# Kernel tuning notes

Measured on AMD Instinct MI355X. Metric: run time of the kernel, lower is better.

## Reference

```python
import jax, jax.numpy as jnp
import numpy as np

H = 256   # hidden_size
D = 256   # embedding_dim
C = 111   # num_classes


def _pos_encoding(L, d):
    pos = jnp.arange(L, dtype=jnp.float32)[:, None]
    div = jnp.exp(jnp.arange(0, d, 2, dtype=jnp.float32) * (-np.log(10000.0) / d))
    pe = jnp.zeros((L, d), dtype=jnp.float32)
    pe = pe.at[:, 0::2].set(jnp.sin(pos * div))
    pe = pe.at[:, 1::2].set(jnp.cos(pos * div))
    return pe


def setup_inputs() -> dict:
    key = jax.random.key(0)
    ks = jax.random.split(key, 12)
    B, Cin, Hh, Ww, T = 64, 1024, 16, 64, 64
    s = 0.02
    return {
        "feature_map": jax.random.normal(ks[0], (B, Cin, Hh, Ww), jnp.float32),
        "count_vector": jax.random.uniform(ks[1], (B, C), jnp.float32),
        "target": jax.random.randint(ks[2], (B, T), 0, C),
        "conv_w": jax.random.normal(ks[3], (2 * H, Cin), jnp.float32) * s,
        "conv_b": jnp.zeros((2 * H,), jnp.float32),
        "emb": jax.random.normal(ks[4], (C, D), jnp.float32) * s,
        "gru_wih": jax.random.normal(ks[5], (3 * H, D + H + C), jnp.float32) * s,
        "gru_whh": jax.random.normal(ks[6], (3 * H, H), jnp.float32) * s,
        "gru_bih": jnp.zeros((3 * H,), jnp.float32),
        "gru_bhh": jnp.zeros((3 * H,), jnp.float32),
        "attn_w": jax.random.normal(ks[7], (H, 2 * H), jnp.float32) * s,
        "attn_b": jnp.zeros((H,), jnp.float32),
        "attn_v": jax.random.normal(ks[8], (1, H), jnp.float32) * s,
        "attn_vb": jnp.zeros((1,), jnp.float32),
        "cov_w": jax.random.normal(ks[9], (H, 1), jnp.float32) * s,
        "cov_b": jnp.zeros((H,), jnp.float32),
        "out_w": jax.random.normal(ks[10], (C, 2 * H + C), jnp.float32) * s,
        "out_b": jnp.zeros((C,), jnp.float32),
    }


def reference(feature_map, count_vector, target, conv_w, conv_b, emb,
              gru_wih, gru_whh, gru_bih, gru_bhh, attn_w, attn_b,
              attn_v, attn_vb, cov_w, cov_b, out_w, out_b):
    B, _, hh, ww = feature_map.shape
    L = hh * ww
    # 1x1 conv + permute to (B, h, w, 2H), add positional encoding, flatten
    feats = jnp.einsum('bchw,oc->bhwo', feature_map, conv_w) + conv_b
    pe = _pos_encoding(L, 2 * H).reshape(hh, ww, 2 * H)
    feats = (feats + pe[None]).reshape(B, L, 2 * H)
    # attention_w(projected_features) is time-invariant -> hoist out of the loop
    Wf = jnp.einsum('bld,hd->blh', feats, attn_w) + attn_b  # (B, L, H)

    # teacher forcing with ratio 1.0: inputs are <sos>=1 then target[:, :-1]
    y_in = jnp.concatenate([jnp.ones((B, 1), target.dtype), target[:, :-1]], axis=1)

    def gru_cell(x, h):  # PyTorch GRUCell math
        gi = x @ gru_wih.T + gru_bih
        gh = h @ gru_whh.T + gru_bhh
        i_r, i_z, i_n = jnp.split(gi, 3, axis=-1)
        h_r, h_z, h_n = jnp.split(gh, 3, axis=-1)
        r = jax.nn.sigmoid(i_r + h_r)
        z = jax.nn.sigmoid(i_z + h_z)
        n = jnp.tanh(i_n + r * h_n)
        return (1.0 - z) * n + z * h

    def step(carry, y_t):
        h, cov = carry  # h: (B,H), cov: (B,L)
        embedded = emb[y_t]
        a = jnp.tanh(Wf + cov[:, :, None] * cov_w[:, 0] + cov_b + h[:, None, :])
        scores = jnp.einsum('blh,h->bl', a, attn_v[0]) + attn_vb[0]
        alpha = jax.nn.softmax(scores, axis=1)
        cov = cov + alpha
        context = jnp.einsum('bl,bld->bd', alpha, feats)[:, :H]
        x = jnp.concatenate([embedded, context, count_vector], axis=1)
        h = gru_cell(x, h)
        out_t = jnp.concatenate([h, context, count_vector], axis=1) @ out_w.T + out_b
        return (h, cov), out_t

    h0 = jnp.zeros((B, H), feats.dtype)
    cov0 = jnp.zeros((B, L), feats.dtype)
    _, outs = jax.lax.scan(step, (h0, cov0), y_in.T)  # (T, B, C)
    return jnp.transpose(outs, (1, 0, 2))
```

## Files before the change

### kernel.cpp

```cpp
#include <hip/hip_runtime.h>
#include <hip/hip_bf16.h>
#include <cstdint>
#include <cstddef>

#define B_   64
#define CIN  1024
#define L_   1024
#define T_   64
#define Hh_  256
#define Dd_  256
#define Cc_  111
#define NO_  512
#define KX_  623

typedef __attribute__((ext_vector_type(8))) short short8;
typedef __attribute__((ext_vector_type(4))) float floatx4;

__device__ __forceinline__ float bf2f(unsigned short u) {
    union { unsigned int i; float f; } v; v.i = ((unsigned int)u) << 16; return v.f;
}
__device__ __forceinline__ unsigned short f2bf(float f) {
    union { float f; unsigned int i; } v; v.f = f;
    return (unsigned short)((v.i + 0x7fffu + ((v.i >> 16) & 1u)) >> 16);
}
__device__ __forceinline__ float frcp(float x) { return __builtin_amdgcn_rcpf(x); }
__device__ __forceinline__ float tanh_fast(float x) {
    return 1.0f - 2.0f * frcp(1.0f + __expf(2.0f * x));
}
__device__ __forceinline__ float sig_fast(float x) {
    return frcp(1.0f + __expf(-x));
}


__global__ void pe_kernel(float* __restrict__ PE) {
    int idx = blockIdx.x * 256 + threadIdx.x;
    if (idx >= L_ * NO_) return;
    int l = idx >> 9, j = idx & 511;
    int i2 = j & ~1;
    float div = expf((float)i2 * (-9.210340371976184f / 512.0f));
    float arg = (float)l * div;
    PE[idx] = (j & 1) ? cosf(arg) : sinf(arg);
}

__global__ void wc_kernel(const float* __restrict__ conv_w,
                          const float* __restrict__ attn_w,
                          unsigned short* __restrict__ Wc) {
    int c = blockIdx.x * 256 + threadIdx.x;
    int o = blockIdx.y;
    float v;
    if (o < 256) {
        v = conv_w[(size_t)o * CIN + c];
    } else {
        const float* aw = attn_w + (size_t)(o - 256) * 512;
        float a = 0.0f;
        for (int d = 0; d < 512; ++d)
            a = fmaf(aw[d], conv_w[(size_t)d * CIN + c], a);
        v = a;
    }
    Wc[(size_t)o * CIN + c] = f2bf(v);
}

__global__ void biasf_kernel(const float* __restrict__ conv_b,
                             const float* __restrict__ PE,
                             float* __restrict__ biasC) {
    int idx = blockIdx.x * 256 + threadIdx.x;
    int l = idx >> 8, j = idx & 255;
    biasC[(size_t)l * NO_ + j] = conv_b[j] + PE[(size_t)l * NO_ + j];
}

__global__ void biasw_kernel(const float* __restrict__ conv_b,
                             const float* __restrict__ PE,
                             const float* __restrict__ attn_w,
                             const float* __restrict__ attn_b,
                             float* __restrict__ biasC) {
    int l = blockIdx.x * 256 + threadIdx.x;
    int h = blockIdx.y;
    const float* aw = attn_w + (size_t)h * 512;
    const float* pe = PE + (size_t)l * NO_;
    float a = 0.0f;
    for (int d = 0; d < 512; ++d)
        a = fmaf(aw[d], conv_b[d] + pe[d], a);
    biasC[(size_t)l * NO_ + 256 + h] = a + attn_b[h];
}

__global__ void wiht_kernel(const float* __restrict__ wih, unsigned short* __restrict__ WihT) {
    int idx = blockIdx.x * 256 + threadIdx.x;
    if (idx >= 768 * KX_) return;
    int o = idx / KX_, k = idx - o * KX_;
    WihT[(size_t)k * 768 + o] = f2bf(wih[idx]);
}
__global__ void whht_kernel(const float* __restrict__ whh, unsigned short* __restrict__ WhhT) {
    int idx = blockIdx.x * 256 + threadIdx.x;
    if (idx >= 768 * 256) return;
    int o = idx >> 8, k = idx & 255;
    WhhT[(size_t)k * 768 + o] = f2bf(whh[idx]);
}
__global__ void woutt_kernel(const float* __restrict__ outw, unsigned short* __restrict__ WoutT) {
    int idx = blockIdx.x * 256 + threadIdx.x;
    if (idx >= Cc_ * KX_) return;
    int c = idx / KX_, k = idx - c * KX_;
    WoutT[(size_t)k * 128 + c] = f2bf(outw[idx]);
}

__global__ void zero_kernel(int* __restrict__ p, int n) {
    int i = blockIdx.x * 256 + threadIdx.x;
    if (i < n) p[i] = 0;
}

__global__ __launch_bounds__(256) void gemm_feats(
    const float* __restrict__ fm,
    const unsigned short* __restrict__ Wc,
    const float* __restrict__ biasC,
    unsigned short* __restrict__ F) {
    __shared__ __align__(16) unsigned short Als[128 * 40];
    __shared__ __align__(16) unsigned short Bls[128 * 40];
    const int tid  = threadIdx.x;
    const int bx   = blockIdx.x;
    const int bb   = bx >> 3;
    const int l0   = (bx & 7) << 7;
    const int n0   = blockIdx.y << 7;
    const int wid  = tid >> 6;
    const int lane = tid & 63;
    const int m0w  = (wid & 1) << 6;
    const int n0w  = (wid >> 1) << 6;
    const int quad = lane >> 4;
    const int l16  = lane & 15;

    floatx4 acc[4][4];
#pragma unroll
    for (int i = 0; i < 4; ++i)
#pragma unroll
        for (int j = 0; j < 4; ++j)
            acc[i][j] = (floatx4){0.f, 0.f, 0.f, 0.f};

    const int lt    = tid & 127;
    const int chalf = tid >> 7;
    const float* fmb = fm + ((size_t)bb * CIN) * L_ + l0 + lt;
    const int bo = tid >> 2;
    const int bc = (tid & 3) << 3;
    const int swzA = ((lt >> 2) & 3) << 3;

    for (int kk = 0; kk < 32; ++kk) {
        const int c0 = kk << 5;
        __syncthreads();
#pragma unroll
        for (int i = 0; i < 8; ++i) {
            int cc = (chalf + (i << 1)) << 1;
            float v0 = fmb[(size_t)(c0 + cc) * L_];
            float v1 = fmb[(size_t)(c0 + cc + 1) * L_];
            unsigned int pk = (unsigned int)f2bf(v0) | ((unsigned int)f2bf(v1) << 16);
            *(unsigned int*)(&Als[lt * 40 + (cc ^ swzA)]) = pk;
        }
#pragma unroll
        for (int i = 0; i < 2; ++i) {
            int o = bo + (i << 6);
            uint4 w = *(const uint4*)(&Wc[(size_t)(n0 + o) * CIN + c0 + bc]);
            *(uint4*)(&Bls[o * 40 + bc]) = w;
        }
        __syncthreads();
        short8 afr[4], bfr[4];
#pragma unroll
        for (int mf = 0; mf < 4; ++mf) {
            int mm = m0w + (mf << 4) + l16;
            int k0 = (quad << 3) ^ (((mm >> 2) & 3) << 3);
            afr[mf] = *(const short8*)(&Als[mm * 40 + k0]);
        }
#pragma unroll
        for (int nf = 0; nf < 4; ++nf) {
            int nn = n0w + (nf << 4) + l16;
            bfr[nf] = *(const short8*)(&Bls[nn * 40 + (quad << 3)]);
        }
#pragma unroll
        for (int mf = 0; mf < 4; ++mf)
#pragma unroll
            for (int nf = 0; nf < 4; ++nf)
                acc[mf][nf] = __builtin_amdgcn_mfma_f32_16x16x32_bf16(afr[mf], bfr[nf], acc[mf][nf], 0, 0, 0);
    }

#pragma unroll
    for (int mf = 0; mf < 4; ++mf) {
#pragma unroll
        for (int nf = 0; nf < 4; ++nf) {
            int colg = n0 + n0w + (nf << 4) + l16;
#pragma unroll
            for (int r = 0; r < 4; ++r) {
                int lb = l0 + m0w + (mf << 4) + (quad << 2) + r;
                float v = acc[mf][nf][r] + biasC[(size_t)lb * NO_ + colg];
                F[((size_t)bb * L_ + lb) * NO_ + colg] = f2bf(v);
            }
        }
    }
}


__device__ __forceinline__ void batch_barrier(int* bar, int target, int tid) {
    __syncthreads();
    if (tid == 0) {
        __hip_atomic_fetch_add(bar, 1, __ATOMIC_RELEASE, __HIP_MEMORY_SCOPE_AGENT);
        while (__hip_atomic_load(bar, __ATOMIC_ACQUIRE, __HIP_MEMORY_SCOPE_AGENT) < target) {
            __builtin_amdgcn_s_sleep(2);
        }
    }
    __syncthreads();
}

__global__ __launch_bounds__(1024, 4) void decoder_kernel(
    const unsigned short* __restrict__ F,
    const unsigned short* __restrict__ WihT,
    const unsigned short* __restrict__ WhhT,
    const unsigned short* __restrict__ WoutT,
    const float* __restrict__ cvv,
    const int* __restrict__ tgt,
    const float* __restrict__ emb,
    const float* __restrict__ bih,
    const float* __restrict__ bhh,
    const float* __restrict__ attn_v,
    const float* __restrict__ attn_vb,
    const float* __restrict__ cov_w,
    const float* __restrict__ cov_b,
    const float* __restrict__ outb,
    int* __restrict__ bar,
    float* __restrict__ gsum,
    float* __restrict__ gctx,
    float* __restrict__ ggih,
    float* __restrict__ OUT) {
    __shared__ __align__(16) unsigned short Wls[256 * 256];
    __shared__ float sc[256];
    __shared__ float cov[256];
    __shared__ float xv[640];
    __shared__ float xo[640];
    __shared__ float hv[256];
    __shared__ __align__(16) float hbs[256];
    __shared__ __align__(16) float cwls[256];
    __shared__ __align__(16) float avls[256];
    __shared__ float gi[768];
    __shared__ float gh[768];
    __shared__ float ctxp[2048];
    __shared__ float outp[1024];
    __shared__ float red[32];

    const int tid  = threadIdx.x;
    const int bx   = blockIdx.x;
    const int b    = bx >> 2;
    const int sub  = bx & 3;
    const int l0   = sub << 8;
    const int lane = tid & 63;
    const int wid  = tid >> 6;
    const int l16  = tid & 15;
    const int lg   = tid >> 4;

    int* mybar = bar + b * 16;

    if (tid < 256) {
        cov[tid] = 0.0f; hv[tid] = 0.0f; hbs[tid] = cov_b[tid];
        cwls[tid] = cov_w[tid]; avls[tid] = attn_v[tid];
    }
    if (tid >= 512 && tid < 512 + Cc_) xv[tid] = cvv[b * Cc_ + (tid - 512)];

    const float avb = attn_vb[0];

#pragma unroll
    for (int i = 0; i < 8; ++i) {
        int c   = (i << 10) + tid;
        int row = c >> 5;
        int col = (c & 31) << 3;
        *(uint4*)(&Wls[(row << 8) + col]) =
            *(const uint4*)(F + (((size_t)(b * L_ + l0 + row)) << 9) + Hh_ + col);
    }

    unsigned int fctx[32];
    {
        const int hp = (tid & 127) << 1;
        const int ch = tid >> 7;
        const unsigned short* fb = F + (((size_t)(b * L_ + l0 + (ch << 5))) << 9) + hp;
#pragma unroll
        for (int i = 0; i < 32; ++i)
            fctx[i] = *(const unsigned int*)(fb + ((size_t)i << 9));
    }

    const int cbase = sub * 28;
    const int ccnt  = (sub == 3) ? 27 : 28;
    const int kg0 = sub * 156;
    const int kg1 = (kg0 + 156 > KX_) ? KX_ : kg0 + 156;
    const int kh0 = sub << 6;

    int nsync = 0;
    __syncthreads();

    for (int t = 0; t < T_; ++t) {
        const int par = t & 1;
        float* myctx = gctx + (((size_t)b * 2 + par) * 4) * 256;
        float* mysum = gsum + ((size_t)b * 2 + par) * 4;
        float* mygg  = ggih + (((size_t)b * 2 + par) * 4) * 1536;

        if (tid < 256) {
            int ytok = (t == 0) ? 1 : tgt[b * T_ + t - 1];
            xv[tid] = emb[ytok * Dd_ + tid];
        }

#pragma unroll
        for (int pass = 0; pass < 4; ++pass) {
            int ll = (pass << 6) + lg;
            float covl = cov[ll];
            const unsigned short* wf = &Wls[ll << 8];
            float a = 0.0f;
#pragma unroll
            for (int j = 0; j < 4; ++j) {
                const int hb0 = (j << 6) + (l16 << 2);
                uint2 w = *(const uint2*)(wf + hb0);
                float4 cw4 = *(const float4*)(&cwls[hb0]);
                float4 av4 = *(const float4*)(&avls[hb0]);
                float4 hb4 = *(const float4*)(&hbs[hb0]);
                float g0 = bf2f((unsigned short)(w.x & 0xffffu)) + fmaf(covl, cw4.x, hb4.x);
                float g1 = bf2f((unsigned short)(w.x >> 16))     + fmaf(covl, cw4.y, hb4.y);
                float g2 = bf2f((unsigned short)(w.y & 0xffffu)) + fmaf(covl, cw4.z, hb4.z);
                float g3 = bf2f((unsigned short)(w.y >> 16))     + fmaf(covl, cw4.w, hb4.w);
                a = fmaf(av4.x, tanh_fast(g0), a);
                a = fmaf(av4.y, tanh_fast(g1), a);
                a = fmaf(av4.z, tanh_fast(g2), a);
                a = fmaf(av4.w, tanh_fast(g3), a);
            }
            a += __shfl_xor(a, 1);
            a += __shfl_xor(a, 2);
            a += __shfl_xor(a, 4);
            a += __shfl_xor(a, 8);
            if (l16 == 0) sc[ll] = __expf(a + avb);
        }
        __syncthreads();

        if (tid < 256) {
            float e = sc[tid];
#pragma unroll
            for (int off = 1; off < 64; off <<= 1) e += __shfl_xor(e, off);
            if (lane == 0) red[wid] = e;
        }

        {
            int hp = (tid & 127) << 1;
            int ch = tid >> 7;
            float c0a = 0.0f, c1a = 0.0f;
#pragma unroll
            for (int i = 0; i < 32; ++i) {
                float al = sc[(ch << 5) + i];
                unsigned int w = fctx[i];
                c0a = fmaf(al, bf2f((unsigned short)(w & 0xffffu)), c0a);
                c1a = fmaf(al, bf2f((unsigned short)(w >> 16)), c1a);
            }
            ctxp[(ch << 8) + hp]     = c0a;
            ctxp[(ch << 8) + hp + 1] = c1a;
        }
        __syncthreads();

        if (tid < 256) {
            float s2 = 0.0f;
#pragma unroll
            for (int i = 0; i < 8; ++i) s2 += ctxp[(i << 8) + tid];
            __hip_atomic_store(&myctx[sub * 256 + tid], s2, __ATOMIC_RELAXED, __HIP_MEMORY_SCOPE_AGENT);
        } else if (tid == 256) {
            float ss = red[0] + red[1] + red[2] + red[3];
            __hip_atomic_store(&mysum[sub], ss, __ATOMIC_RELAXED, __HIP_MEMORY_SCOPE_AGENT);
        }

        ++nsync;
        batch_barrier(mybar, 4 * nsync, tid);

        float s2 = 0.0f;
        if (tid < 256) {
#pragma unroll
            for (int s = 0; s < 4; ++s)
                s2 += __hip_atomic_load(&myctx[s * 256 + tid], __ATOMIC_RELAXED, __HIP_MEMORY_SCOPE_AGENT);
        } else if (tid == 256) {
            float S = 0.0f;
#pragma unroll
            for (int s = 0; s < 4; ++s)
                S += __hip_atomic_load(&mysum[s], __ATOMIC_RELAXED, __HIP_MEMORY_SCOPE_AGENT);
            red[16] = frcp(S);
        }
        __syncthreads();
        float rS = red[16];
        if (tid < 256) {
            xv[256 + tid] = s2 * rS;
            cov[tid] += sc[tid] * rS;
        }
        __syncthreads();

        if (tid < 384) {
            int o = tid << 1;
            float a0 = 0.0f, a1 = 0.0f;
            const unsigned short* wp = WihT + o;
            for (int k = kg0; k < kg1; ++k) {
                float x = xv[k];
                unsigned int w = *(const unsigned int*)(wp + (size_t)k * 768);
                a0 = fmaf(x, bf2f((unsigned short)(w & 0xffffu)), a0);
                a1 = fmaf(x, bf2f((unsigned short)(w >> 16)), a1);
            }
            __hip_atomic_store(&mygg[sub * 1536 + o],     a0, __ATOMIC_RELAXED, __HIP_MEMORY_SCOPE_AGENT);
            __hip_atomic_store(&mygg[sub * 1536 + o + 1], a1, __ATOMIC_RELAXED, __HIP_MEMORY_SCOPE_AGENT);
        } else if (tid < 768) {
            int o = (tid - 384) << 1;
            float a0 = 0.0f, a1 = 0.0f;
            const unsigned short* wp = WhhT + o;
            for (int k = kh0; k < kh0 + 64; ++k) {
                float x = hv[k];
                unsigned int w = *(const unsigned int*)(wp + (size_t)k * 768);
                a0 = fmaf(x, bf2f((unsigned short)(w & 0xffffu)), a0);
                a1 = fmaf(x, bf2f((unsigned short)(w >> 16)), a1);
            }
            __hip_atomic_store(&mygg[sub * 1536 + 768 + o],     a0, __ATOMIC_RELAXED, __HIP_MEMORY_SCOPE_AGENT);
            __hip_atomic_store(&mygg[sub * 1536 + 768 + o + 1], a1, __ATOMIC_RELAXED, __HIP_MEMORY_SCOPE_AGENT);
        }

        ++nsync;
        batch_barrier(mybar, 4 * nsync, tid);

        if (tid < 384) {
            int o = tid << 1;
            float v0 = bih[o], v1 = bih[o + 1];
#pragma unroll
            for (int s = 0; s < 4; ++s) {
                v0 += __hip_atomic_load(&mygg[s * 1536 + o],     __ATOMIC_RELAXED, __HIP_MEMORY_SCOPE_AGENT);
                v1 += __hip_atomic_load(&mygg[s * 1536 + o + 1], __ATOMIC_RELAXED, __HIP_MEMORY_SCOPE_AGENT);
            }
            gi[o] = v0; gi[o + 1] = v1;
        } else if (tid < 768) {
            int o = (tid - 384) << 1;
            float v0 = bhh[o], v1 = bhh[o + 1];
#pragma unroll
            for (int s = 0; s < 4; ++s) {
                v0 += __hip_atomic_load(&mygg[s * 1536 + 768 + o],     __ATOMIC_RELAXED, __HIP_MEMORY_SCOPE_AGENT);
                v1 += __hip_atomic_load(&mygg[s * 1536 + 768 + o + 1], __ATOMIC_RELAXED, __HIP_MEMORY_SCOPE_AGENT);
            }
            gh[o] = v0; gh[o + 1] = v1;
        }
        __syncthreads();

        if (tid < 256) {
            float r = sig_fast(gi[tid] + gh[tid]);
            float z = sig_fast(gi[256 + tid] + gh[256 + tid]);
            float n = tanh_fast(fmaf(r, gh[512 + tid], gi[512 + tid]));
            float hold = hv[tid];
            float hn = (1.0f - z) * n + z * hold;
            hv[tid] = hn;
            hbs[tid] = hn + cov_b[tid];
            xo[tid] = hn;
        } else if (tid < KX_) {
            xo[tid] = xv[tid];
        }
        __syncthreads();

        {
            int cc = tid & 31;
            int ch = tid >> 5;
            int k0 = ch * 20;
            int k1 = k0 + 20; if (k1 > KX_) k1 = KX_;
            float a = 0.0f;
            for (int k = k0; k < k1; ++k)
                a = fmaf(xo[k], bf2f(WoutT[(size_t)k * 128 + cbase + cc]), a);
            outp[(ch << 5) + cc] = a;
        }
        __syncthreads();
        if (tid < ccnt) {
            float s3 = outb[cbase + tid];
#pragma unroll
            for (int i = 0; i < 32; ++i) s3 += outp[(i << 5) + tid];
            OUT[((size_t)b * T_ + t) * Cc_ + cbase + tid] = s3;
        }
        __syncthreads();
    }
}

extern "C" void kernel_launch(void* const* d_in, const int* in_sizes, int n_in,
                              void* d_out, int out_size, void* d_ws, size_t ws_size,
                              hipStream_t stream) {
    const float* fm      = (const float*)d_in[0];
    const float* cvv     = (const float*)d_in[1];
    const int*   tgt     = (const int*)d_in[2];
    const float* conv_w  = (const float*)d_in[3];
    const float* conv_b  = (const float*)d_in[4];
    const float* emb     = (const float*)d_in[5];
    const float* wih     = (const float*)d_in[6];
    const float* whh     = (const float*)d_in[7];
    const float* bih     = (const float*)d_in[8];
    const float* bhh     = (const float*)d_in[9];
    const float* attn_w  = (const float*)d_in[10];
    const float* attn_b  = (const float*)d_in[11];
    const float* attn_v  = (const float*)d_in[12];
    const float* attn_vb = (const float*)d_in[13];
    const float* cov_w   = (const float*)d_in[14];
    const float* cov_b   = (const float*)d_in[15];
    const float* outw    = (const float*)d_in[16];
    const float* outb    = (const float*)d_in[17];
    float* OUT = (float*)d_out;
    char* ws = (char*)d_ws;

    unsigned short* F     = (unsigned short*)(ws);
    unsigned short* Wc    = (unsigned short*)(ws + 67108864);
    float*          biasC = (float*)(ws + 68157440);
    float*          PE    = (float*)(ws + 70254592);
    unsigned short* WihT  = (unsigned short*)(ws + 72351744);
    unsigned short* WhhT  = (unsigned short*)(ws + 73308672);
    unsigned short* WoutT = (unsigned short*)(ws + 73701888);

    int*   bar  = (int*)(ws + 68157440);
    float* gsum = (float*)(ws + 68161536);
    float* gctx = (float*)(ws + 68165632);
    float* ggih = (float*)(ws + 68689920);

    pe_kernel<<<2048, 256, 0, stream>>>(PE);
    wc_kernel<<<dim3(4, 512), 256, 0, stream>>>(conv_w, attn_w, Wc);
    biasf_kernel<<<1024, 256, 0, stream>>>(conv_b, PE, biasC);
    biasw_kernel<<<dim3(4, 256), 256, 0, stream>>>(conv_b, PE, attn_w, attn_b, biasC);
    wiht_kernel<<<1869, 256, 0, stream>>>(wih, WihT);
    whht_kernel<<<768, 256, 0, stream>>>(whh, WhhT);
    woutt_kernel<<<271, 256, 0, stream>>>(outw, WoutT);
    gemm_feats<<<dim3(512, 4), 256, 0, stream>>>(fm, Wc, biasC, F);
    zero_kernel<<<4, 256, 0, stream>>>(bar, 1024);
    decoder_kernel<<<256, 1024, 0, stream>>>(F, WihT, WhhT, WoutT,
        cvv, tgt, emb, bih, bhh, attn_v, attn_vb, cov_w, cov_b, outb,
        bar, gsum, gctx, ggih, OUT);
}
```

Baseline: 3.300 ms.

## Cache output weights in registers, prefetch embeddings, remap blocks, relax barrier spin

Several changes to the decoder loop. The output-projection weight slice is held in registers for all timesteps, target tokens are cached in shared memory and the next embedding row is prefetched one step ahead, and the GRU matvec loops use pointer increments with unroll 4. Blocks are remapped so the four sub-blocks of one batch item sit eight apart in launch order, the barrier spin load is relaxed, and output stores are nontemporal. The aim is to cut global load latency on the serial per-step path. The costs are extra register pressure under launch_bounds(1024,4) and possible memory-ordering risk from the relaxed spin.

```diff
diff --git a/kernel.cpp b/kernel.cpp
--- a/kernel.cpp
+++ b/kernel.cpp
@@ -197,7 +197,7 @@
     __syncthreads();
     if (tid == 0) {
         __hip_atomic_fetch_add(bar, 1, __ATOMIC_RELEASE, __HIP_MEMORY_SCOPE_AGENT);
-        while (__hip_atomic_load(bar, __ATOMIC_ACQUIRE, __HIP_MEMORY_SCOPE_AGENT) < target) {
+        while (__hip_atomic_load(bar, __ATOMIC_RELAXED, __HIP_MEMORY_SCOPE_AGENT) < target) {
             __builtin_amdgcn_s_sleep(2);
         }
     }
@@ -238,11 +238,13 @@
     __shared__ float ctxp[2048];
     __shared__ float outp[1024];
     __shared__ float red[32];
+    __shared__ int   tok[T_];
 
     const int tid  = threadIdx.x;
-    const int bx   = blockIdx.x;
-    const int b    = bx >> 2;
-    const int sub  = bx & 3;
+    const int bxr  = blockIdx.x;
+    const int q_   = bxr >> 3;
+    const int sub  = q_ & 3;
+    const int b    = (bxr & 7) | ((q_ >> 2) << 3);
     const int l0   = sub << 8;
     const int lane = tid & 63;
     const int wid  = tid >> 6;
@@ -256,6 +258,8 @@
         cwls[tid] = cov_w[tid]; avls[tid] = attn_v[tid];
     }
     if (tid >= 512 && tid < 512 + Cc_) xv[tid] = cvv[b * Cc_ + (tid - 512)];
+    if (tid >= KX_ && tid < 640) xo[tid] = 0.0f;
+    if (tid < T_) tok[tid] = (tid == 0) ? 1 : tgt[b * T_ + tid - 1];
 
     const float avb = attn_vb[0];
 
@@ -284,8 +288,21 @@
     const int kg1 = (kg0 + 156 > KX_) ? KX_ : kg0 + 156;
     const int kh0 = sub << 6;
 
+    unsigned short wout_r[20];
+    {
+        int cc = tid & 31, ch = tid >> 5, k0 = ch * 20;
+#pragma unroll
+        for (int i = 0; i < 20; ++i) {
+            int k = k0 + i;
+            wout_r[i] = (k < KX_) ? WoutT[(size_t)k * 128 + cbase + cc] : (unsigned short)0;
+        }
+    }
+
     int nsync = 0;
     __syncthreads();
+
+    float ecur = 0.0f;
+    if (tid < 256) ecur = emb[(size_t)tok[0] * Dd_ + tid];
 
     for (int t = 0; t < T_; ++t) {
         const int par = t & 1;
@@ -294,8 +311,8 @@
         float* mygg  = ggih + (((size_t)b * 2 + par) * 4) * 1536;
 
         if (tid < 256) {
-            int ytok = (t == 0) ? 1 : tgt[b * T_ + t - 1];
-            xv[tid] = emb[ytok * Dd_ + tid];
+            xv[tid] = ecur;
+            if (t + 1 < T_) ecur = emb[(size_t)tok[t + 1] * Dd_ + tid];
         }
 
 #pragma unroll
@@ -387,10 +404,12 @@
         if (tid < 384) {
             int o = tid << 1;
             float a0 = 0.0f, a1 = 0.0f;
-            const unsigned short* wp = WihT + o;
+            const unsigned short* wp = WihT + (size_t)kg0 * 768 + o;
+#pragma unroll 4
             for (int k = kg0; k < kg1; ++k) {
                 float x = xv[k];
-                unsigned int w = *(const unsigned int*)(wp + (size_t)k * 768);
+                unsigned int w = *(const unsigned int*)wp;
+                wp += 768;
                 a0 = fmaf(x, bf2f((unsigned short)(w & 0xffffu)), a0);
                 a1 = fmaf(x, bf2f((unsigned short)(w >> 16)), a1);
             }
@@ -399,10 +418,12 @@
         } else if (tid < 768) {
             int o = (tid - 384) << 1;
             float a0 = 0.0f, a1 = 0.0f;
-            const unsigned short* wp = WhhT + o;
+            const unsigned short* wp = WhhT + (size_t)kh0 * 768 + o;
+#pragma unroll 4
             for (int k = kh0; k < kh0 + 64; ++k) {
                 float x = hv[k];
-                unsigned int w = *(const unsigned int*)(wp + (size_t)k * 768);
+                unsigned int w = *(const unsigned int*)wp;
+                wp += 768;
                 a0 = fmaf(x, bf2f((unsigned short)(w & 0xffffu)), a0);
                 a1 = fmaf(x, bf2f((unsigned short)(w >> 16)), a1);
             }
@@ -449,21 +470,20 @@
         __syncthreads();
 
         {
-            int cc = tid & 31;
             int ch = tid >> 5;
             int k0 = ch * 20;
-            int k1 = k0 + 20; if (k1 > KX_) k1 = KX_;
             float a = 0.0f;
-            for (int k = k0; k < k1; ++k)
-                a = fmaf(xo[k], bf2f(WoutT[(size_t)k * 128 + cbase + cc]), a);
-            outp[(ch << 5) + cc] = a;
+#pragma unroll
+            for (int i = 0; i < 20; ++i)
+                a = fmaf(xo[k0 + i], bf2f(wout_r[i]), a);
+            outp[tid] = a;
         }
         __syncthreads();
         if (tid < ccnt) {
             float s3 = outb[cbase + tid];
 #pragma unroll
             for (int i = 0; i < 32; ++i) s3 += outp[(i << 5) + tid];
-            OUT[((size_t)b * T_ + t) * Cc_ + cbase + tid] = s3;
+            __builtin_nontemporal_store(s3, &OUT[((size_t)b * T_ + t) * Cc_ + cbase + tid]);
         }
         __syncthreads();
     }
```

Result: faster. 2.857 ms (-13.4%).
